# Kernel tuning notes

Hardware: AMD Instinct MI355X
Metric: run time of the kernel (lower is better)

Reference implementation:

```python
import jax, jax.numpy as jnp
import numpy as np

D_MODEL = 1024
N_HEADS = 16
DEPTH = D_MODEL // N_HEADS
B, S = 2, 2048


def layer_norm(x, gamma, beta):
    # Faithful to the torch module: unbiased std (ddof=1), eps added to std.
    mean = jnp.mean(x, axis=-1, keepdims=True)
    std = jnp.std(x, axis=-1, ddof=1, keepdims=True)
    return gamma * ((x - mean) / (std + 1e-6)) + beta


def setup_inputs() -> dict:
    key = jax.random.key(0)
    ks = jax.random.split(key, 12)
    sc = 0.02
    x = jax.random.normal(ks[0], (B, S, D_MODEL), jnp.float32)
    mask = jnp.triu(jnp.ones((S, S), jnp.float32), k=1)  # 1 where masked (future)
    return {
        "x": x,
        "mask": mask,
        "wq_w": jax.random.normal(ks[1], (D_MODEL, D_MODEL), jnp.float32) * sc,
        "wq_b": jnp.zeros((D_MODEL,), jnp.float32),
        "wk_w": jax.random.normal(ks[2], (D_MODEL, D_MODEL), jnp.float32) * sc,
        "wk_b": jnp.zeros((D_MODEL,), jnp.float32),
        "wv_w": jax.random.normal(ks[3], (D_MODEL, D_MODEL), jnp.float32) * sc,
        "wv_b": jnp.zeros((D_MODEL,), jnp.float32),
        "dense_w": jax.random.normal(ks[4], (D_MODEL, D_MODEL), jnp.float32) * sc,
        "dense_b": jnp.zeros((D_MODEL,), jnp.float32),
        "gamma1": jnp.ones((D_MODEL,), jnp.float32),
        "beta1": jnp.zeros((D_MODEL,), jnp.float32),
        "gamma2": jnp.ones((D_MODEL,), jnp.float32),
        "beta2": jnp.zeros((D_MODEL,), jnp.float32),
        "fc_w": jax.random.normal(ks[5], (4 * D_MODEL, D_MODEL), jnp.float32) * sc,
        "proj_w": jax.random.normal(ks[6], (D_MODEL, 4 * D_MODEL), jnp.float32) * sc,
    }


def reference(x, mask, wq_w, wq_b, wk_w, wk_b, wv_w, wv_b, dense_w, dense_b,
              gamma1, beta1, gamma2, beta2, fc_w, proj_w):
    # x: [B,S,D]. Dropout is identity in eval.
    xn = layer_norm(x, gamma1, beta1)

    def split(h):  # [B,S,D] -> [B,H,S,depth]
        return h.reshape(B, S, N_HEADS, DEPTH).transpose(0, 2, 1, 3)

    q = split(xn @ wq_w.T + wq_b)
    k = split(xn @ wk_w.T + wk_b)
    v = split(xn @ wv_w.T + wv_b)

    scores = jnp.einsum("bhqd,bhkd->bhqk", q, k) / jnp.sqrt(
        jnp.asarray(DEPTH, jnp.float32))
    scores = scores + mask * -1e9
    attn = jax.nn.softmax(scores, axis=-1)
    ctx = jnp.einsum("bhqk,bhkd->bhqd", attn, v)
    ctx = ctx.transpose(0, 2, 1, 3).reshape(B, S, D_MODEL)
    attn_out = ctx @ dense_w.T + dense_b

    # Residual adds the *normed* x (faithful to the original ordering).
    h = xn + attn_out
    hn = layer_norm(h, gamma2, beta2)

    ff = jax.nn.gelu(hn @ fc_w.T, approximate=False) @ proj_w.T
    return hn + ff
```

## Files before the change

kernel.cpp:

```cpp
#include <hip/hip_runtime.h>
#include <math.h>

typedef __bf16 bf16;
typedef __attribute__((ext_vector_type(2))) __bf16 bf16x2;
typedef __attribute__((ext_vector_type(4))) __bf16 bf16x4;
typedef __attribute__((ext_vector_type(8))) __bf16 bf16x8;
typedef __attribute__((ext_vector_type(4))) float f32x4;

#define D_MODEL 1024
#define NH 16
#define DP 64
#define BB 2
#define SEQ 2048
#define TOK 4096
#define FFD 4096
#define AST 72

__device__ __forceinline__ void async16(bf16* lds, const bf16* g) {
    __builtin_amdgcn_global_load_lds(
        (__attribute__((address_space(1))) void*)g,
        (__attribute__((address_space(3))) void*)lds, 16, 0, 0);
}

__device__ __forceinline__ f32x4 mfma16(bf16x8 a, bf16x8 b, f32x4 c) {
    return __builtin_amdgcn_mfma_f32_16x16x32_bf16(a, b, c, 0, 0, 0);
}

__global__ __launch_bounds__(256) void cvt_w(
    const float4* __restrict__ in, bf16x4* __restrict__ out, int n4)
{
    const int i = blockIdx.x * 256 + threadIdx.x;
    if (i >= n4) return;
    const float4 v = in[i];
    bf16x4 o; o[0] = (bf16)v.x; o[1] = (bf16)v.y; o[2] = (bf16)v.z; o[3] = (bf16)v.w;
    out[i] = o;
}

template<typename TIN>
__global__ __launch_bounds__(256) void ln_kernel(
    const TIN* __restrict__ in, const float* __restrict__ g,
    const float* __restrict__ be, bf16* __restrict__ out)
{
    const size_t row = blockIdx.x;
    const int t = threadIdx.x;
    const TIN* x = in + row * D_MODEL;

    float v0, v1, v2, v3;
    if constexpr (sizeof(TIN) == 4) {
        const float4 xv = *(const float4*)(x + t * 4);
        v0 = xv.x; v1 = xv.y; v2 = xv.z; v3 = xv.w;
    } else {
        const bf16x4 xv = *(const bf16x4*)(x + t * 4);
        v0 = (float)xv[0]; v1 = (float)xv[1]; v2 = (float)xv[2]; v3 = (float)xv[3];
    }
    float s  = v0 + v1 + v2 + v3;
    float ss = v0*v0 + v1*v1 + v2*v2 + v3*v3;
    #pragma unroll
    for (int off = 32; off > 0; off >>= 1) {
        s  += __shfl_down(s, off);
        ss += __shfl_down(ss, off);
    }
    __shared__ float rs[4], rss[4];
    if ((t & 63) == 0) { rs[t >> 6] = s; rss[t >> 6] = ss; }
    __syncthreads();
    const float S  = rs[0] + rs[1] + rs[2] + rs[3];
    const float SS = rss[0] + rss[1] + rss[2] + rss[3];
    const float mean = S * (1.0f / 1024.0f);
    const float var  = fmaxf((SS - S * mean) * (1.0f / 1023.0f), 0.0f);
    const float inv  = 1.0f / (sqrtf(var) + 1e-6f);

    const float4 gv = *(const float4*)(g  + t * 4);
    const float4 bv = *(const float4*)(be + t * 4);
    bf16x4 ov;
    ov[0] = (bf16)(gv.x * ((v0 - mean) * inv) + bv.x);
    ov[1] = (bf16)(gv.y * ((v1 - mean) * inv) + bv.y);
    ov[2] = (bf16)(gv.z * ((v2 - mean) * inv) + bv.z);
    ov[3] = (bf16)(gv.w * ((v3 - mean) * inv) + bv.w);
    *(bf16x4*)(out + row * D_MODEL + t * 4) = ov;
}

template<int EPI, typename TOUT>
__global__ __launch_bounds__(256, 2) void gemm_bt(
    const bf16* __restrict__ A, const bf16* __restrict__ W,
    const float* __restrict__ bias, const bf16* res,
    TOUT* C, int M, int N, int K, float scale)
{
    __shared__ __align__(16) bf16 As[128 * 32];
    __shared__ __align__(16) bf16 Bs[128 * 32];
    const int t = threadIdx.x;
    const int w = t >> 6, lane = t & 63;
    const int fr = lane & 15, quad = lane >> 4;
    const int m0 = blockIdx.y * 128, n0 = blockIdx.x * 128;
    const int wm = (w >> 1) * 64, wn = (w & 1) * 64;

    const f32x4 z = {0.f, 0.f, 0.f, 0.f};
    f32x4 acc[4][4];
    #pragma unroll
    for (int i = 0; i < 4; ++i)
        #pragma unroll
        for (int j = 0; j < 4; ++j) acc[i][j] = z;

    const int nk = K >> 5;
    for (int kt = 0; kt < nk; ++kt) {
        const int k0 = kt << 5;
        #pragma unroll
        for (int call = 0; call < 2; ++call) {
            const int c = call * 256 + t;
            const int row = c >> 2, sub = c & 3;
            async16(&As[(size_t)(call * 256 + w * 64) * 8],
                    A + (size_t)(m0 + row) * K + k0 + sub * 8);
            async16(&Bs[(size_t)(call * 256 + w * 64) * 8],
                    W + (size_t)(n0 + row) * K + k0 + sub * 8);
        }
        __syncthreads();
        bf16x8 af[4], bfr[4];
        #pragma unroll
        for (int i = 0; i < 4; ++i)
            af[i] = *(const bf16x8*)&As[(wm + i * 16 + fr) * 32 + quad * 8];
        #pragma unroll
        for (int j = 0; j < 4; ++j)
            bfr[j] = *(const bf16x8*)&Bs[(wn + j * 16 + fr) * 32 + quad * 8];
        #pragma unroll
        for (int i = 0; i < 4; ++i)
            #pragma unroll
            for (int j = 0; j < 4; ++j)
                acc[i][j] = mfma16(af[i], bfr[j], acc[i][j]);
        __syncthreads();
    }

    #pragma unroll
    for (int i = 0; i < 4; ++i) {
        #pragma unroll
        for (int j = 0; j < 4; ++j) {
            #pragma unroll
            for (int r = 0; r < 4; ++r) {
                const int m = m0 + wm + i * 16 + quad * 4 + r;
                const int n = n0 + wn + j * 16 + fr;
                float v = acc[i][j][r];
                if (EPI == 1) {
                    v += bias[n];
                    v += (float)res[(size_t)m * N + n];
                    C[(size_t)m * N + n] = (TOUT)v;
                } else if (EPI == 2) {
                    v = 0.5f * v * (1.0f + erff(v * 0.70710678118f));
                    C[(size_t)m * N + n] = (TOUT)v;
                } else {
                    v += (float)res[(size_t)m * N + n];
                    C[(size_t)m * N + n] = (TOUT)v;
                }
            }
        }
    }
}

__global__ __launch_bounds__(256, 2) void gemm_qkv(
    const bf16* __restrict__ A,
    const bf16* __restrict__ wq, const bf16* __restrict__ wk,
    const bf16* __restrict__ wvv,
    const float* __restrict__ bq, const float* __restrict__ bk,
    const float* __restrict__ bv,
    bf16* __restrict__ outq, bf16* __restrict__ outk, bf16* __restrict__ outv)
{
    const int sel = blockIdx.x >> 3;
    const bf16* W = (sel == 0) ? wq : ((sel == 1) ? wk : wvv);
    const float* bias = (sel == 0) ? bq : ((sel == 1) ? bk : bv);
    bf16* C = (sel == 0) ? outq : ((sel == 1) ? outk : outv);
    const float scale = (sel == 0) ? 0.125f : 1.0f;
    const int K = D_MODEL;

    __shared__ __align__(16) bf16 As[128 * 32];
    __shared__ __align__(16) bf16 Bs[128 * 32];
    const int t = threadIdx.x;
    const int w = t >> 6, lane = t & 63;
    const int fr = lane & 15, quad = lane >> 4;
    const int m0 = blockIdx.y * 128, n0 = (blockIdx.x & 7) * 128;
    const int wm = (w >> 1) * 64, wn = (w & 1) * 64;

    const f32x4 z = {0.f, 0.f, 0.f, 0.f};
    f32x4 acc[4][4];
    #pragma unroll
    for (int i = 0; i < 4; ++i)
        #pragma unroll
        for (int j = 0; j < 4; ++j) acc[i][j] = z;

    for (int kt = 0; kt < (D_MODEL >> 5); ++kt) {
        const int k0 = kt << 5;
        #pragma unroll
        for (int call = 0; call < 2; ++call) {
            const int c = call * 256 + t;
            const int row = c >> 2, sub = c & 3;
            async16(&As[(size_t)(call * 256 + w * 64) * 8],
                    A + (size_t)(m0 + row) * K + k0 + sub * 8);
            async16(&Bs[(size_t)(call * 256 + w * 64) * 8],
                    W + (size_t)(n0 + row) * K + k0 + sub * 8);
        }
        __syncthreads();
        bf16x8 af[4], bfr[4];
        #pragma unroll
        for (int i = 0; i < 4; ++i)
            af[i] = *(const bf16x8*)&As[(wm + i * 16 + fr) * 32 + quad * 8];
        #pragma unroll
        for (int j = 0; j < 4; ++j)
            bfr[j] = *(const bf16x8*)&Bs[(wn + j * 16 + fr) * 32 + quad * 8];
        #pragma unroll
        for (int i = 0; i < 4; ++i)
            #pragma unroll
            for (int j = 0; j < 4; ++j)
                acc[i][j] = mfma16(af[i], bfr[j], acc[i][j]);
        __syncthreads();
    }

    #pragma unroll
    for (int i = 0; i < 4; ++i)
        #pragma unroll
        for (int j = 0; j < 4; ++j)
            #pragma unroll
            for (int r = 0; r < 4; ++r) {
                const int m = m0 + wm + i * 16 + quad * 4 + r;
                const int n = n0 + wn + j * 16 + fr;
                const float vv = (acc[i][j][r] + bias[n]) * scale;
                const int b = m >> 11, s = m & 2047, h = n >> 6, d = n & 63;
                C[(((size_t)(b * NH + h)) * SEQ + s) * DP + d] = (bf16)vv;
            }
}

__global__ __launch_bounds__(256, 2) void attn_kernel(
    const bf16* __restrict__ q, const bf16* __restrict__ k,
    const bf16* __restrict__ v, bf16* __restrict__ ctx)
{
    __shared__ __align__(16) bf16 Ks[2][64 * AST];
    __shared__ __align__(16) bf16 VsT[2][64 * AST];
    __shared__ __align__(16) bf16 Ps[4][16 * AST];
    const int t = threadIdx.x, wv = t >> 6, lane = t & 63;
    const int fr = lane & 15, quad = lane >> 4;
    const int bh = blockIdx.y;
    const size_t base = (size_t)bh * SEQ * DP;
    const int b = bh >> 4, hh = bh & 15;
    const f32x4 z = {0.f, 0.f, 0.f, 0.f};
    const int krow = t >> 2, kd0 = (t & 3) * 16;
    const int pp = t & 31, c0 = (t >> 5) * 8;

    for (int half = 0; half < 2; ++half) {
        const int qt = half ? (31 - (int)blockIdx.x) : (int)blockIdx.x;
        const int q0 = qt * 64, qr0 = q0 + wv * 16;
        const int nkt = qt + 1;

        __syncthreads();

        bf16x8 qf[2];
        #pragma unroll
        for (int c = 0; c < 2; ++c)
            qf[c] = *(const bf16x8*)(q + base + (size_t)(qr0 + fr) * DP + c * 32 + quad * 8);

        bf16x8 k0r, k1r, v0r, v1r;
        {
            const bf16* kp = k + base + (size_t)krow * DP + kd0;
            k0r = *(const bf16x8*)kp; k1r = *(const bf16x8*)(kp + 8);
            const bf16* vp = v + base + (size_t)(2 * pp) * DP + c0;
            v0r = *(const bf16x8*)vp; v1r = *(const bf16x8*)(vp + DP);
        }

        f32x4 o[4] = {z, z, z, z};
        float mi[4] = {-1e30f, -1e30f, -1e30f, -1e30f};
        float li[4] = {0.f, 0.f, 0.f, 0.f};

        for (int kt = 0; kt < nkt; ++kt) {
            const int cur = kt & 1;
            const int kk0 = kt * 64;
            *(bf16x8*)&Ks[cur][krow * AST + kd0]     = k0r;
            *(bf16x8*)&Ks[cur][krow * AST + kd0 + 8] = k1r;
            #pragma unroll
            for (int j = 0; j < 8; ++j) {
                bf16x2 pr; pr[0] = v0r[j]; pr[1] = v1r[j];
                *(bf16x2*)&VsT[cur][(c0 + j) * AST + 2 * pp] = pr;
            }
            __syncthreads();
            if (kt + 1 < nkt) {
                const bf16* kp = k + base + (size_t)(kk0 + 64 + krow) * DP + kd0;
                k0r = *(const bf16x8*)kp; k1r = *(const bf16x8*)(kp + 8);
                const bf16* vp = v + base + (size_t)(kk0 + 64 + 2 * pp) * DP + c0;
                v0r = *(const bf16x8*)vp; v1r = *(const bf16x8*)(vp + DP);
            }

            f32x4 sa[4] = {z, z, z, z};
            #pragma unroll
            for (int nb = 0; nb < 4; ++nb)
                #pragma unroll
                for (int c = 0; c < 2; ++c) {
                    const bf16x8 kf = *(const bf16x8*)&Ks[cur][(nb * 16 + fr) * AST + c * 32 + quad * 8];
                    sa[nb] = mfma16(qf[c], kf, sa[nb]);
                }

            float p[4][4], rmax[4];
            #pragma unroll
            for (int r = 0; r < 4; ++r) rmax[r] = -1e30f;
            #pragma unroll
            for (int nb = 0; nb < 4; ++nb)
                #pragma unroll
                for (int r = 0; r < 4; ++r) {
                    const int key = kk0 + nb * 16 + fr;
                    const int qrow = qr0 + quad * 4 + r;
                    float sv = sa[nb][r];
                    if (key > qrow) sv += -1e9f;
                    p[nb][r] = sv;
                    rmax[r] = fmaxf(rmax[r], sv);
                }
            #pragma unroll
            for (int off = 1; off < 16; off <<= 1)
                #pragma unroll
                for (int r = 0; r < 4; ++r)
                    rmax[r] = fmaxf(rmax[r], __shfl_xor(rmax[r], off));

            float alpha[4], psum[4];
            #pragma unroll
            for (int r = 0; r < 4; ++r) {
                const float nm = fmaxf(mi[r], rmax[r]);
                alpha[r] = __expf(mi[r] - nm);
                mi[r] = nm;
                float ps = 0.f;
                #pragma unroll
                for (int nb = 0; nb < 4; ++nb) {
                    const float e = __expf(p[nb][r] - nm);
                    p[nb][r] = e;
                    ps += e;
                }
                psum[r] = ps;
            }
            #pragma unroll
            for (int off = 1; off < 16; off <<= 1)
                #pragma unroll
                for (int r = 0; r < 4; ++r)
                    psum[r] += __shfl_xor(psum[r], off);
            #pragma unroll
            for (int r = 0; r < 4; ++r) li[r] = li[r] * alpha[r] + psum[r];
            #pragma unroll
            for (int db = 0; db < 4; ++db)
                #pragma unroll
                for (int r = 0; r < 4; ++r) o[db][r] *= alpha[r];

            #pragma unroll
            for (int nb = 0; nb < 4; ++nb)
                #pragma unroll
                for (int r = 0; r < 4; ++r)
                    Ps[wv][(quad * 4 + r) * AST + nb * 16 + fr] = (bf16)p[nb][r];

            bf16x8 pf[2];
            #pragma unroll
            for (int c = 0; c < 2; ++c)
                pf[c] = *(const bf16x8*)&Ps[wv][fr * AST + c * 32 + quad * 8];
            #pragma unroll
            for (int db = 0; db < 4; ++db)
                #pragma unroll
                for (int c = 0; c < 2; ++c) {
                    const bf16x8 vf = *(const bf16x8*)&VsT[cur][(db * 16 + fr) * AST + c * 32 + quad * 8];
                    o[db] = mfma16(pf[c], vf, o[db]);
                }
        }

        #pragma unroll
        for (int db = 0; db < 4; ++db)
            #pragma unroll
            for (int r = 0; r < 4; ++r) {
                const int qrow = qr0 + quad * 4 + r;
                const int d = db * 16 + fr;
                ctx[((size_t)(b * SEQ + qrow)) * D_MODEL + hh * DP + d] =
                    (bf16)(o[db][r] / li[r]);
            }
    }
}

extern "C" void kernel_launch(void* const* d_in, const int* in_sizes, int n_in,
                              void* d_out, int out_size, void* d_ws, size_t ws_size,
                              hipStream_t stream) {
    const float* x       = (const float*)d_in[0];
    const float* wq_w    = (const float*)d_in[2];
    const float* wq_b    = (const float*)d_in[3];
    const float* wk_w    = (const float*)d_in[4];
    const float* wk_b    = (const float*)d_in[5];
    const float* wv_w    = (const float*)d_in[6];
    const float* wv_b    = (const float*)d_in[7];
    const float* dense_w = (const float*)d_in[8];
    const float* dense_b = (const float*)d_in[9];
    const float* gamma1  = (const float*)d_in[10];
    const float* beta1   = (const float*)d_in[11];
    const float* gamma2  = (const float*)d_in[12];
    const float* beta2   = (const float*)d_in[13];
    const float* fc_w    = (const float*)d_in[14];
    const float* proj_w  = (const float*)d_in[15];
    float* out = (float*)d_out;

    bf16* ws = (bf16*)d_ws;
    const size_t M1 = (size_t)1 << 20;
    bf16* xn   = ws;
    bf16* qb   = ws + 4 * M1;
    bf16* kb   = ws + 8 * M1;
    bf16* vb   = ws + 12 * M1;
    bf16* ctx  = ws + 16 * M1;
    bf16* ff1  = qb;
    bf16* wqc  = ws + 20 * M1;
    bf16* wkc  = ws + 21 * M1;
    bf16* wvc  = ws + 22 * M1;
    bf16* wdc  = ws + 23 * M1;
    bf16* fcc  = ws + 24 * M1;
    bf16* prjc = ws + 28 * M1;
    bf16* h = xn, *hn = xn;

    cvt_w<<<1024, 256, 0, stream>>>((const float4*)wq_w,    (bf16x4*)wqc,  1 << 18);
    cvt_w<<<1024, 256, 0, stream>>>((const float4*)wk_w,    (bf16x4*)wkc,  1 << 18);
    cvt_w<<<1024, 256, 0, stream>>>((const float4*)wv_w,    (bf16x4*)wvc,  1 << 18);
    cvt_w<<<1024, 256, 0, stream>>>((const float4*)dense_w, (bf16x4*)wdc,  1 << 18);
    cvt_w<<<4096, 256, 0, stream>>>((const float4*)fc_w,    (bf16x4*)fcc,  1 << 20);
    cvt_w<<<4096, 256, 0, stream>>>((const float4*)proj_w,  (bf16x4*)prjc, 1 << 20);

    ln_kernel<float><<<TOK, 256, 0, stream>>>(x, gamma1, beta1, xn);
    gemm_qkv<<<dim3(24, 32), 256, 0, stream>>>(xn, wqc, wkc, wvc,
                                               wq_b, wk_b, wv_b, qb, kb, vb);
    attn_kernel<<<dim3(16, BB * NH), 256, 0, stream>>>(qb, kb, vb, ctx);
    gemm_bt<1, bf16><<<dim3(8, 32), 256, 0, stream>>>(ctx, wdc, dense_b, xn, h,
                                                      TOK, D_MODEL, D_MODEL, 1.0f);
    ln_kernel<bf16><<<TOK, 256, 0, stream>>>(h, gamma2, beta2, hn);
    gemm_bt<2, bf16><<<dim3(32, 32), 256, 0, stream>>>(hn, fcc, nullptr, nullptr, ff1,
                                                       TOK, FFD, D_MODEL, 1.0f);
    gemm_bt<3, float><<<dim3(8, 32), 256, 0, stream>>>(ff1, prjc, nullptr, hn, out,
                                                       TOK, D_MODEL, FFD, 1.0f);
}
```

Measured before the change: 414.4 us.

## Merge weight conversions into one launch; use 128x64 tiles for N=1024 GEMMs

Replaces the six separate weight-conversion launches with a single kernel that indexes into a six-segment pointer table, which removes launch overhead. Adds a gemm_bt64 variant with 128x64 output tiles, used for the dense projection and the FFN down-projection (N=1024), so these GEMMs launch 512 blocks instead of 256 and fill the GPU's compute units better. The trade-off is more reloading of A tiles from memory and a smaller tile of MFMA work per wave.

```diff
diff --git a/kernel.cpp b/kernel.cpp
--- a/kernel.cpp
+++ b/kernel.cpp
@@ -26,14 +26,22 @@
     return __builtin_amdgcn_mfma_f32_16x16x32_bf16(a, b, c, 0, 0, 0);
 }
 
-__global__ __launch_bounds__(256) void cvt_w(
-    const float4* __restrict__ in, bf16x4* __restrict__ out, int n4)
+struct CvtArgs {
+    const float4* in[6];
+    bf16x4* out[6];
+};
+__global__ __launch_bounds__(256) void cvt_all(CvtArgs a)
 {
     const int i = blockIdx.x * 256 + threadIdx.x;
-    if (i >= n4) return;
-    const float4 v = in[i];
+    int seg, idx;
+    if (i < (1 << 20)) { seg = i >> 18; idx = i & ((1 << 18) - 1); }
+    else {
+        const int j = i - (1 << 20);
+        seg = 4 + (j >> 20); idx = j & ((1 << 20) - 1);
+    }
+    const float4 v = a.in[seg][idx];
     bf16x4 o; o[0] = (bf16)v.x; o[1] = (bf16)v.y; o[2] = (bf16)v.z; o[3] = (bf16)v.w;
-    out[i] = o;
+    a.out[seg][idx] = o;
 }
 
 template<typename TIN>
@@ -143,6 +151,80 @@
                     C[(size_t)m * N + n] = (TOUT)v;
                 } else if (EPI == 2) {
                     v = 0.5f * v * (1.0f + erff(v * 0.70710678118f));
+                    C[(size_t)m * N + n] = (TOUT)v;
+                } else {
+                    v += (float)res[(size_t)m * N + n];
+                    C[(size_t)m * N + n] = (TOUT)v;
+                }
+            }
+        }
+    }
+}
+
+template<int EPI, typename TOUT>
+__global__ __launch_bounds__(256, 2) void gemm_bt64(
+    const bf16* __restrict__ A, const bf16* __restrict__ W,
+    const float* __restrict__ bias, const bf16* res,
+    TOUT* C, int M, int N, int K)
+{
+    __shared__ __align__(16) bf16 As[128 * 32];
+    __shared__ __align__(16) bf16 Bs[64 * 32];
+    const int t = threadIdx.x;
+    const int w = t >> 6, lane = t & 63;
+    const int fr = lane & 15, quad = lane >> 4;
+    const int m0 = blockIdx.y * 128, n0 = blockIdx.x * 64;
+    const int wm = (w >> 1) * 64, wn = (w & 1) * 32;
+
+    const f32x4 z = {0.f, 0.f, 0.f, 0.f};
+    f32x4 acc[4][2];
+    #pragma unroll
+    for (int i = 0; i < 4; ++i)
+        #pragma unroll
+        for (int j = 0; j < 2; ++j) acc[i][j] = z;
+
+    const int nk = K >> 5;
+    for (int kt = 0; kt < nk; ++kt) {
+        const int k0 = kt << 5;
+        #pragma unroll
+        for (int call = 0; call < 2; ++call) {
+            const int c = call * 256 + t;
+            const int row = c >> 2, sub = c & 3;
+            async16(&As[(size_t)(call * 256 + w * 64) * 8],
+                    A + (size_t)(m0 + row) * K + k0 + sub * 8);
+        }
+        {
+            const int row = t >> 2, sub = t & 3;
+            async16(&Bs[(size_t)(w * 64) * 8],
+                    W + (size_t)(n0 + row) * K + k0 + sub * 8);
+        }
+        __syncthreads();
+        bf16x8 af[4], bfr[2];
+        #pragma unroll
+        for (int i = 0; i < 4; ++i)
+            af[i] = *(const bf16x8*)&As[(wm + i * 16 + fr) * 32 + quad * 8];
+        #pragma unroll
+        for (int j = 0; j < 2; ++j)
+            bfr[j] = *(const bf16x8*)&Bs[(wn + j * 16 + fr) * 32 + quad * 8];
+        #pragma unroll
+        for (int i = 0; i < 4; ++i)
+            #pragma unroll
+            for (int j = 0; j < 2; ++j)
+                acc[i][j] = mfma16(af[i], bfr[j], acc[i][j]);
+        __syncthreads();
+    }
+
+    #pragma unroll
+    for (int i = 0; i < 4; ++i) {
+        #pragma unroll
+        for (int j = 0; j < 2; ++j) {
+            #pragma unroll
+            for (int r = 0; r < 4; ++r) {
+                const int m = m0 + wm + i * 16 + quad * 4 + r;
+                const int n = n0 + wn + j * 16 + fr;
+                float v = acc[i][j][r];
+                if (EPI == 1) {
+                    v += bias[n];
+                    v += (float)res[(size_t)m * N + n];
                     C[(size_t)m * N + n] = (TOUT)v;
                 } else {
                     v += (float)res[(size_t)m * N + n];
@@ -405,22 +487,24 @@
     bf16* prjc = ws + 28 * M1;
     bf16* h = xn, *hn = xn;
 
-    cvt_w<<<1024, 256, 0, stream>>>((const float4*)wq_w,    (bf16x4*)wqc,  1 << 18);
-    cvt_w<<<1024, 256, 0, stream>>>((const float4*)wk_w,    (bf16x4*)wkc,  1 << 18);
-    cvt_w<<<1024, 256, 0, stream>>>((const float4*)wv_w,    (bf16x4*)wvc,  1 << 18);
-    cvt_w<<<1024, 256, 0, stream>>>((const float4*)dense_w, (bf16x4*)wdc,  1 << 18);
-    cvt_w<<<4096, 256, 0, stream>>>((const float4*)fc_w,    (bf16x4*)fcc,  1 << 20);
-    cvt_w<<<4096, 256, 0, stream>>>((const float4*)proj_w,  (bf16x4*)prjc, 1 << 20);
+    CvtArgs ca;
+    ca.in[0] = (const float4*)wq_w;    ca.out[0] = (bf16x4*)wqc;
+    ca.in[1] = (const float4*)wk_w;    ca.out[1] = (bf16x4*)wkc;
+    ca.in[2] = (const float4*)wv_w;    ca.out[2] = (bf16x4*)wvc;
+    ca.in[3] = (const float4*)dense_w; ca.out[3] = (bf16x4*)wdc;
+    ca.in[4] = (const float4*)fc_w;    ca.out[4] = (bf16x4*)fcc;
+    ca.in[5] = (const float4*)proj_w;  ca.out[5] = (bf16x4*)prjc;
+    cvt_all<<<12288, 256, 0, stream>>>(ca);
 
     ln_kernel<float><<<TOK, 256, 0, stream>>>(x, gamma1, beta1, xn);
     gemm_qkv<<<dim3(24, 32), 256, 0, stream>>>(xn, wqc, wkc, wvc,
                                                wq_b, wk_b, wv_b, qb, kb, vb);
     attn_kernel<<<dim3(16, BB * NH), 256, 0, stream>>>(qb, kb, vb, ctx);
-    gemm_bt<1, bf16><<<dim3(8, 32), 256, 0, stream>>>(ctx, wdc, dense_b, xn, h,
-                                                      TOK, D_MODEL, D_MODEL, 1.0f);
+    gemm_bt64<1, bf16><<<dim3(16, 32), 256, 0, stream>>>(ctx, wdc, dense_b, xn, h,
+                                                         TOK, D_MODEL, D_MODEL);
     ln_kernel<bf16><<<TOK, 256, 0, stream>>>(h, gamma2, beta2, hn);
     gemm_bt<2, bf16><<<dim3(32, 32), 256, 0, stream>>>(hn, fcc, nullptr, nullptr, ff1,
                                                        TOK, FFD, D_MODEL, 1.0f);
-    gemm_bt<3, float><<<dim3(8, 32), 256, 0, stream>>>(ff1, prjc, nullptr, hn, out,
-                                                       TOK, D_MODEL, FFD, 1.0f);
-}
+    gemm_bt64<3, float><<<dim3(16, 32), 256, 0, stream>>>(ff1, prjc, nullptr, hn, out,
+                                                          TOK, D_MODEL, FFD);
+}
```

Result: faster. 394.4 us (-4.8%).
